# Kernel optimization log

Hardware: AMD Instinct MI355X
Metric: run time of the kernel (lower is better)

The kernel has to match this reference:

```python
import jax, jax.numpy as jnp
import numpy as np

C, W, H = 16, 48, 48
OUTDIMS = 4000
COMPONENTS = 1
BATCH = 128
EPS = 1e-6
INIT_NOISE = 1e-3


def setup_inputs() -> dict:
    key = jax.random.key(0)
    kx, kw, kh, kf = jax.random.split(key, 4)
    x = jax.random.normal(kx, (BATCH, C, W, H), dtype=jnp.float32)
    width = jax.random.normal(kw, (OUTDIMS, 1, W, 1, COMPONENTS), dtype=jnp.float32) * INIT_NOISE
    height = jax.random.normal(kh, (OUTDIMS, 1, 1, H, COMPONENTS), dtype=jnp.float32) * INIT_NOISE
    features = jax.random.normal(kf, (OUTDIMS, C, 1, 1), dtype=jnp.float32) * INIT_NOISE
    bias = jnp.zeros((OUTDIMS,), dtype=jnp.float32)
    return {"x": x, "width": width, "height": height, "features": features, "bias": bias}


def reference(x, width, height, features, bias):
    # normalize width over the w axis (dim 2), height over the h axis (dim 3)
    wn = width / jnp.sqrt(jnp.sum(width * width, axis=2, keepdims=True) + EPS)
    hn = height / jnp.sqrt(jnp.sum(height * height, axis=3, keepdims=True) + EPS)
    # spatial mask: sum of outer products over components -> (outdims, w, h)
    spatial = jnp.sum(wn * hn, axis=4)[:, 0]  # broadcast (n,1,w,1,k)*(n,1,1,h,k)
    feat = features[:, :, 0, 0]  # (outdims, c)
    # y[b,n] = sum_{c,w,h} x[b,c,w,h] * spatial[n,w,h] * feat[n,c]  (same math as
    # x.view(N,-1) @ weight.t() where weight = spatial * features, flattened cwh)
    y = jnp.einsum('bcwh,nwh,nc->bn', x, spatial, feat)
    return y + bias[None, :]
```

## Files before the change

### kernel.cpp

```cpp
#include <hip/hip_runtime.h>
#include <stdint.h>

#define OUTD 4000
#define NPAD 4096
#define CC 16
#define WW 48
#define HH 48
#define BB 128
#define KD 768
#define MD 6144
#define EPSF 1e-6f

#define BM 192
#define BN 128
#define BK 64
#define KSTEPS 12
#define THREADS 512
#define XPB 2304

using short8 = __attribute__((ext_vector_type(8))) short;
using f32x4  = __attribute__((ext_vector_type(4))) float;

static __device__ __forceinline__ unsigned short f2bf(float f) {
  union { float f; unsigned int u; } v; v.f = f;
  unsigned int u = v.u;
  unsigned int r = (u + 0x7FFFu + ((u >> 16) & 1u)) >> 16;
  return (unsigned short)r;
}

__global__ __launch_bounds__(256)
void prep_all(const float* __restrict__ x,
              const float* __restrict__ width,
              const float* __restrict__ height,
              const float* __restrict__ feat,
              unsigned short* __restrict__ A,
              unsigned short* __restrict__ Qt,
              float* __restrict__ wnT) {
  __shared__ float smw[4][WW];
  int bid = blockIdx.x;
  if (bid < XPB) {
    int t = bid * 256 + threadIdx.x;
    int e = t * 8;
    int h0 = e % HH;
    int w = (e / HH) % WW;
    int c = (e / (HH * WW)) % CC;
    int b = e / (HH * WW * CC);
    float4 v0 = *(const float4*)(x + e);
    float4 v1 = *(const float4*)(x + e + 4);
    short8 o;
    o[0] = (short)f2bf(v0.x); o[1] = (short)f2bf(v0.y);
    o[2] = (short)f2bf(v0.z); o[3] = (short)f2bf(v0.w);
    o[4] = (short)f2bf(v1.x); o[5] = (short)f2bf(v1.y);
    o[6] = (short)f2bf(v1.z); o[7] = (short)f2bf(v1.w);
    *(short8*)&A[(size_t)(b * WW + w) * KD + c * HH + h0] = o;
  } else {
    int lane = threadIdx.x & 63;
    int wv = threadIdx.x >> 6;
    int nbase = (bid - XPB) * 4;
    int n = nbase + wv;
    bool valid = (n < OUTD);
    float hv = (valid && lane < HH) ? height[n * HH + lane] : 0.f;
    float wvv = (valid && lane < WW) ? width[n * WW + lane] : 0.f;
    float hs = hv * hv, wsum = wvv * wvv;
    #pragma unroll
    for (int off = 32; off > 0; off >>= 1) {
      hs += __shfl_xor(hs, off);
      wsum += __shfl_xor(wsum, off);
    }
    float hnorm = rsqrtf(hs + EPSF);
    float wnorm = rsqrtf(wsum + EPSF);
    if (lane < WW) smw[wv][lane] = wvv * wnorm;
    if (valid) {
      #pragma unroll
      for (int i = lane; i < KD; i += 64) {
        int c = i / HH, h = i % HH;
        Qt[(size_t)n * KD + i] = f2bf(feat[n * CC + c] * height[n * HH + h] * hnorm);
      }
    } else {
      #pragma unroll
      for (int i = lane; i < KD; i += 64) Qt[(size_t)n * KD + i] = 0;
    }
    __syncthreads();
    if (threadIdx.x < WW) {
      int w = threadIdx.x;
      float4 o = make_float4(smw[0][w], smw[1][w], smw[2][w], smw[3][w]);
      *(float4*)&wnT[w * NPAD + nbase] = o;
    }
  }
}

__global__ __launch_bounds__(THREADS, 2)
void gemm_main(const unsigned short* __restrict__ A,
               const unsigned short* __restrict__ Qt,
               const float* __restrict__ wnT,
               const float* __restrict__ bias,
               float* __restrict__ out) {
  __shared__ unsigned short S[3][(BM + BN) * BK];

  int tid = threadIdx.x;
  int lane = tid & 63;
  int wid = tid >> 6;
  int wm = wid >> 1;
  int wnh = wid & 1;

  int bid = blockIdx.x;
  int xcd = bid & 7;
  int idx = bid >> 3;
  int by = xcd * 4 + (idx & 3);
  int bx = idx >> 2;
  int n0 = bx * BN;
  int m0 = by * BM;

  int rsub = lane >> 3;
  int kswb = ((lane & 7) ^ rsub) * 8;
  const unsigned short* gA[3];
  const unsigned short* gB[2];
  #pragma unroll
  for (int j = 0; j < 3; ++j)
    gA[j] = A + (size_t)(m0 + (wid * 3 + j) * 8 + rsub) * KD + kswb;
  #pragma unroll
  for (int j = 0; j < 2; ++j)
    gB[j] = Qt + (size_t)(n0 + (wid * 2 + j) * 8 + rsub) * KD + kswb;

#define STAGE_A(ks, buf)                                                         \
  { _Pragma("unroll")                                                            \
    for (int j = 0; j < 3; ++j)                                                  \
      __builtin_amdgcn_global_load_lds(                                          \
          (const __attribute__((address_space(1))) void*)(gA[j] + (ks) * BK),    \
          (__attribute__((address_space(3))) void*)(&S[buf][(wid * 3 + j) * 512]), \
          16, 0, 0); }
#define STAGE_B(ks, buf)                                                         \
  { _Pragma("unroll")                                                            \
    for (int j = 0; j < 2; ++j)                                                  \
      __builtin_amdgcn_global_load_lds(                                          \
          (const __attribute__((address_space(1))) void*)(gB[j] + (ks) * BK),    \
          (__attribute__((address_space(3))) void*)(&S[buf][BM * BK + (wid * 2 + j) * 512]), \
          16, 0, 0); }

  int q16 = lane & 15;
  int hi = lane >> 4;
  int q7 = q16 & 7;
  int aofs[2], bofs[2];
  #pragma unroll
  for (int kc = 0; kc < 2; ++kc) {
    aofs[kc] = (wm * 48 + q16) * BK + (((kc * 4 + hi) ^ q7) * 8);
    bofs[kc] = BM * BK + (wnh * 64 + q16) * BK + (((kc * 4 + hi) ^ q7) * 8);
  }

  f32x4 acc[3][4] = {};

  STAGE_A(0, 0); STAGE_B(0, 0);
  STAGE_A(1, 1); STAGE_B(1, 1);
  asm volatile("s_waitcnt vmcnt(5)" ::: "memory");
  __builtin_amdgcn_s_barrier();
  __builtin_amdgcn_sched_barrier(0);

  #pragma unroll
  for (int ks = 0; ks < KSTEPS; ++ks) {
    const unsigned short* sb = &S[ks % 3][0];
    short8 af0, af1, af2;
    #pragma unroll
    for (int kc = 0; kc < 2; ++kc) {
      #pragma unroll
      for (int nh = 0; nh < 2; ++nh) {
        if (nh == 0) {
          af0 = *(const short8*)&sb[aofs[kc]];
          af1 = *(const short8*)&sb[aofs[kc] + 16 * BK];
          af2 = *(const short8*)&sb[aofs[kc] + 32 * BK];
        }
        short8 b0 = *(const short8*)&sb[bofs[kc] + (nh * 2) * 16 * BK];
        short8 b1 = *(const short8*)&sb[bofs[kc] + (nh * 2 + 1) * 16 * BK];
        if (ks + 2 < KSTEPS) {
          if (kc == 0 && nh == 0) STAGE_A(ks + 2, (ks + 2) % 3);
          if (kc == 0 && nh == 1) STAGE_B(ks + 2, (ks + 2) % 3);
        }
        __builtin_amdgcn_s_barrier();
        asm volatile("s_waitcnt lgkmcnt(0)" ::: "memory");
        __builtin_amdgcn_sched_barrier(0);
        __builtin_amdgcn_s_setprio(1);
        acc[0][nh * 2]     = __builtin_amdgcn_mfma_f32_16x16x32_bf16(af0, b0, acc[0][nh * 2], 0, 0, 0);
        acc[1][nh * 2]     = __builtin_amdgcn_mfma_f32_16x16x32_bf16(af1, b0, acc[1][nh * 2], 0, 0, 0);
        acc[2][nh * 2]     = __builtin_amdgcn_mfma_f32_16x16x32_bf16(af2, b0, acc[2][nh * 2], 0, 0, 0);
        acc[0][nh * 2 + 1] = __builtin_amdgcn_mfma_f32_16x16x32_bf16(af0, b1, acc[0][nh * 2 + 1], 0, 0, 0);
        acc[1][nh * 2 + 1] = __builtin_amdgcn_mfma_f32_16x16x32_bf16(af1, b1, acc[1][nh * 2 + 1], 0, 0, 0);
        acc[2][nh * 2 + 1] = __builtin_amdgcn_mfma_f32_16x16x32_bf16(af2, b1, acc[2][nh * 2 + 1], 0, 0, 0);
        __builtin_amdgcn_s_setprio(0);
        if (kc == 1 && nh == 1) {
          if (ks <= KSTEPS - 3)      asm volatile("s_waitcnt vmcnt(5)" ::: "memory");
          else if (ks == KSTEPS - 2) asm volatile("s_waitcnt vmcnt(0)" ::: "memory");
        }
        __builtin_amdgcn_s_barrier();
        __builtin_amdgcn_sched_barrier(0);
      }
    }
  }

  int b = by * 4 + wm;
  #pragma unroll
  for (int ni = 0; ni < 4; ++ni) {
    int ng = n0 + wnh * 64 + ni * 16 + q16;
    float sum = 0.f;
    #pragma unroll
    for (int mi = 0; mi < 3; ++mi) {
      int wbase = mi * 16 + hi * 4;
      f32x4 v = acc[mi][ni];
      #pragma unroll
      for (int r = 0; r < 4; ++r)
        sum += wnT[(wbase + r) * NPAD + ng] * v[r];
    }
    sum += __shfl_xor(sum, 16);
    sum += __shfl_xor(sum, 32);
    if (hi == 0 && ng < OUTD)
      out[(size_t)b * OUTD + ng] = sum + bias[ng];
  }
#undef STAGE_A
#undef STAGE_B
}

extern "C" void kernel_launch(void* const* d_in, const int* in_sizes, int n_in,
                              void* d_out, int out_size, void* d_ws, size_t ws_size,
                              hipStream_t stream) {
  const float* x      = (const float*)d_in[0];
  const float* width  = (const float*)d_in[1];
  const float* height = (const float*)d_in[2];
  const float* feat   = (const float*)d_in[3];
  const float* bias   = (const float*)d_in[4];
  float* out = (float*)d_out;

  char* ws = (char*)d_ws;
  unsigned short* A  = (unsigned short*)ws;
  unsigned short* Qt = (unsigned short*)(ws + 9437184);
  float* wnT         = (float*)(ws + 9437184 + 6291456);

  prep_all<<<dim3(XPB + NPAD / 4), dim3(256), 0, stream>>>(x, width, height, feat, A, Qt, wnT);
  gemm_main<<<dim3(1024), dim3(THREADS), 0, stream>>>(A, Qt, wnT, bias, out);
}
```

Measured before the change: 59.59 us.

## Double GEMM M-tile to 384 and use 4-slot BK=32 pipeline

Doubles the M tile per block from 192 to 384 rows (two batch samples per warp row), halving the grid to 512 blocks so each B tile is reused across more rows. The K loop is restructured into 24 units of BK=32 with a 4-deep LDS ring buffer, prefetching 3 units ahead and using one barrier per unit instead of several. The LDS swizzle and epilogue change to match, and the epilogue writes two output rows per warp. The cost is more accumulator registers (24 f32x4 per wave) and fewer blocks, which risks lower occupancy and a worse tail on 256 CUs.

```diff
diff --git a/kernel.cpp b/kernel.cpp
--- a/kernel.cpp
+++ b/kernel.cpp
@@ -11,10 +11,11 @@
 #define MD 6144
 #define EPSF 1e-6f
 
-#define BM 192
+#define BM 384
 #define BN 128
-#define BK 64
-#define KSTEPS 12
+#define BKU 32
+#define UNITS 24
+#define SLOT_ELEMS ((BM + BN) * BKU)
 #define THREADS 512
 #define XPB 2304
 
@@ -95,7 +96,7 @@
                const float* __restrict__ wnT,
                const float* __restrict__ bias,
                float* __restrict__ out) {
-  __shared__ unsigned short S[3][(BM + BN) * BK];
+  __shared__ unsigned short S[4 * SLOT_ELEMS];
 
   int tid = threadIdx.x;
   int lane = tid & 63;
@@ -105,116 +106,136 @@
 
   int bid = blockIdx.x;
   int xcd = bid & 7;
-  int idx = bid >> 3;
-  int by = xcd * 4 + (idx & 3);
-  int bx = idx >> 2;
+  int i = bid >> 3;
+  int by = xcd * 2 + (i & 1);
+  int bx = i >> 1;
   int n0 = bx * BN;
   int m0 = by * BM;
 
-  int rsub = lane >> 3;
-  int kswb = ((lane & 7) ^ rsub) * 8;
-  const unsigned short* gA[3];
-  const unsigned short* gB[2];
-  #pragma unroll
-  for (int j = 0; j < 3; ++j)
-    gA[j] = A + (size_t)(m0 + (wid * 3 + j) * 8 + rsub) * KD + kswb;
-  #pragma unroll
-  for (int j = 0; j < 2; ++j)
-    gB[j] = Qt + (size_t)(n0 + (wid * 2 + j) * 8 + rsub) * KD + kswb;
-
-#define STAGE_A(ks, buf)                                                         \
-  { _Pragma("unroll")                                                            \
-    for (int j = 0; j < 3; ++j)                                                  \
-      __builtin_amdgcn_global_load_lds(                                          \
-          (const __attribute__((address_space(1))) void*)(gA[j] + (ks) * BK),    \
-          (__attribute__((address_space(3))) void*)(&S[buf][(wid * 3 + j) * 512]), \
-          16, 0, 0); }
-#define STAGE_B(ks, buf)                                                         \
-  { _Pragma("unroll")                                                            \
-    for (int j = 0; j < 2; ++j)                                                  \
-      __builtin_amdgcn_global_load_lds(                                          \
-          (const __attribute__((address_space(1))) void*)(gB[j] + (ks) * BK),    \
-          (__attribute__((address_space(3))) void*)(&S[buf][BM * BK + (wid * 2 + j) * 512]), \
-          16, 0, 0); }
+  int lrow = lane >> 2;
+  int g = lane & 3;
+  int gsw = (g ^ ((lrow >> 1) & 3)) * 8;
+  const unsigned short* gA0 = A + (size_t)(m0 + (wid * 3 + 0) * 16 + lrow) * KD + gsw;
+  const unsigned short* gA1 = A + (size_t)(m0 + (wid * 3 + 1) * 16 + lrow) * KD + gsw;
+  const unsigned short* gA2 = A + (size_t)(m0 + (wid * 3 + 2) * 16 + lrow) * KD + gsw;
+  const unsigned short* gB0 = Qt + (size_t)(n0 + wid * 16 + lrow) * KD + gsw;
+  int aD0 = (wid * 3 + 0) * 512;
+  int aD1 = (wid * 3 + 1) * 512;
+  int aD2 = (wid * 3 + 2) * 512;
+  int bD  = BM * BKU + wid * 512;
+
+#define SLOTB(u) (((u) & 3) * SLOT_ELEMS)
+#define STAGE(u)                                                                  \
+  { __builtin_amdgcn_global_load_lds(                                             \
+        (const __attribute__((address_space(1))) void*)(gA0 + (u) * BKU),         \
+        (__attribute__((address_space(3))) void*)(&S[SLOTB(u) + aD0]), 16, 0, 0); \
+    __builtin_amdgcn_global_load_lds(                                             \
+        (const __attribute__((address_space(1))) void*)(gA1 + (u) * BKU),         \
+        (__attribute__((address_space(3))) void*)(&S[SLOTB(u) + aD1]), 16, 0, 0); \
+    __builtin_amdgcn_global_load_lds(                                             \
+        (const __attribute__((address_space(1))) void*)(gA2 + (u) * BKU),         \
+        (__attribute__((address_space(3))) void*)(&S[SLOTB(u) + aD2]), 16, 0, 0); \
+    __builtin_amdgcn_global_load_lds(                                             \
+        (const __attribute__((address_space(1))) void*)(gB0 + (u) * BKU),         \
+        (__attribute__((address_space(3))) void*)(&S[SLOTB(u) + bD]), 16, 0, 0); }
 
   int q16 = lane & 15;
   int hi = lane >> 4;
-  int q7 = q16 & 7;
-  int aofs[2], bofs[2];
+  int kq = (q16 >> 1) & 3;
+  int aoff = (wm * 96 + q16) * BKU + (hi ^ kq) * 8;
+  int boff = BM * BKU + (wnh * 64 + q16) * BKU + (hi ^ kq) * 8;
+
+  f32x4 acc[6][4] = {};
+
+  STAGE(0); STAGE(1); STAGE(2);
+
   #pragma unroll
-  for (int kc = 0; kc < 2; ++kc) {
-    aofs[kc] = (wm * 48 + q16) * BK + (((kc * 4 + hi) ^ q7) * 8);
-    bofs[kc] = BM * BK + (wnh * 64 + q16) * BK + (((kc * 4 + hi) ^ q7) * 8);
+  for (int u = 0; u < UNITS; ++u) {
+    if (u + 3 < UNITS) STAGE(u + 3);
+    __builtin_amdgcn_sched_barrier(0);
+    if (u <= UNITS - 4)      asm volatile("s_waitcnt vmcnt(12)" ::: "memory");
+    else if (u == UNITS - 3) asm volatile("s_waitcnt vmcnt(8)" ::: "memory");
+    else if (u == UNITS - 2) asm volatile("s_waitcnt vmcnt(4)" ::: "memory");
+    else                     asm volatile("s_waitcnt vmcnt(0)" ::: "memory");
+    __builtin_amdgcn_s_barrier();
+    __builtin_amdgcn_sched_barrier(0);
+
+    const unsigned short* sb = &S[SLOTB(u)];
+    short8 af0 = *(const short8*)&sb[aoff];
+    short8 af1 = *(const short8*)&sb[aoff + 512];
+    short8 af2 = *(const short8*)&sb[aoff + 1024];
+    short8 af3 = *(const short8*)&sb[aoff + 1536];
+    short8 af4 = *(const short8*)&sb[aoff + 2048];
+    short8 af5 = *(const short8*)&sb[aoff + 2560];
+    short8 bf0 = *(const short8*)&sb[boff];
+    short8 bf1 = *(const short8*)&sb[boff + 512];
+    asm volatile("s_waitcnt lgkmcnt(0)" ::: "memory");
+    __builtin_amdgcn_sched_barrier(0);
+    __builtin_amdgcn_s_setprio(1);
+    acc[0][0] = __builtin_amdgcn_mfma_f32_16x16x32_bf16(af0, bf0, acc[0][0], 0, 0, 0);
+    acc[1][0] = __builtin_amdgcn_mfma_f32_16x16x32_bf16(af1, bf0, acc[1][0], 0, 0, 0);
+    acc[2][0] = __builtin_amdgcn_mfma_f32_16x16x32_bf16(af2, bf0, acc[2][0], 0, 0, 0);
+    acc[3][0] = __builtin_amdgcn_mfma_f32_16x16x32_bf16(af3, bf0, acc[3][0], 0, 0, 0);
+    acc[4][0] = __builtin_amdgcn_mfma_f32_16x16x32_bf16(af4, bf0, acc[4][0], 0, 0, 0);
+    acc[5][0] = __builtin_amdgcn_mfma_f32_16x16x32_bf16(af5, bf0, acc[5][0], 0, 0, 0);
+    acc[0][1] = __builtin_amdgcn_mfma_f32_16x16x32_bf16(af0, bf1, acc[0][1], 0, 0, 0);
+    acc[1][1] = __builtin_amdgcn_mfma_f32_16x16x32_bf16(af1, bf1, acc[1][1], 0, 0, 0);
+    acc[2][1] = __builtin_amdgcn_mfma_f32_16x16x32_bf16(af2, bf1, acc[2][1], 0, 0, 0);
+    acc[3][1] = __builtin_amdgcn_mfma_f32_16x16x32_bf16(af3, bf1, acc[3][1], 0, 0, 0);
+    acc[4][1] = __builtin_amdgcn_mfma_f32_16x16x32_bf16(af4, bf1, acc[4][1], 0, 0, 0);
+    acc[5][1] = __builtin_amdgcn_mfma_f32_16x16x32_bf16(af5, bf1, acc[5][1], 0, 0, 0);
+    __builtin_amdgcn_s_setprio(0);
+    __builtin_amdgcn_sched_barrier(0);
+
+    short8 bf2 = *(const short8*)&sb[boff + 1024];
+    short8 bf3 = *(const short8*)&sb[boff + 1536];
+    asm volatile("s_waitcnt lgkmcnt(0)" ::: "memory");
+    __builtin_amdgcn_sched_barrier(0);
+    __builtin_amdgcn_s_setprio(1);
+    acc[0][2] = __builtin_amdgcn_mfma_f32_16x16x32_bf16(af0, bf2, acc[0][2], 0, 0, 0);
+    acc[1][2] = __builtin_amdgcn_mfma_f32_16x16x32_bf16(af1, bf2, acc[1][2], 0, 0, 0);
+    acc[2][2] = __builtin_amdgcn_mfma_f32_16x16x32_bf16(af2, bf2, acc[2][2], 0, 0, 0);
+    acc[3][2] = __builtin_amdgcn_mfma_f32_16x16x32_bf16(af3, bf2, acc[3][2], 0, 0, 0);
+    acc[4][2] = __builtin_amdgcn_mfma_f32_16x16x32_bf16(af4, bf2, acc[4][2], 0, 0, 0);
+    acc[5][2] = __builtin_amdgcn_mfma_f32_16x16x32_bf16(af5, bf2, acc[5][2], 0, 0, 0);
+    acc[0][3] = __builtin_amdgcn_mfma_f32_16x16x32_bf16(af0, bf3, acc[0][3], 0, 0, 0);
+    acc[1][3] = __builtin_amdgcn_mfma_f32_16x16x32_bf16(af1, bf3, acc[1][3], 0, 0, 0);
+    acc[2][3] = __builtin_amdgcn_mfma_f32_16x16x32_bf16(af2, bf3, acc[2][3], 0, 0, 0);
+    acc[3][3] = __builtin_amdgcn_mfma_f32_16x16x32_bf16(af3, bf3, acc[3][3], 0, 0, 0);
+    acc[4][3] = __builtin_amdgcn_mfma_f32_16x16x32_bf16(af4, bf3, acc[4][3], 0, 0, 0);
+    acc[5][3] = __builtin_amdgcn_mfma_f32_16x16x32_bf16(af5, bf3, acc[5][3], 0, 0, 0);
+    __builtin_amdgcn_s_setprio(0);
+    __builtin_amdgcn_s_barrier();
+    __builtin_amdgcn_sched_barrier(0);
   }
 
-  f32x4 acc[3][4] = {};
-
-  STAGE_A(0, 0); STAGE_B(0, 0);
-  STAGE_A(1, 1); STAGE_B(1, 1);
-  asm volatile("s_waitcnt vmcnt(5)" ::: "memory");
-  __builtin_amdgcn_s_barrier();
-  __builtin_amdgcn_sched_barrier(0);
-
-  #pragma unroll
-  for (int ks = 0; ks < KSTEPS; ++ks) {
-    const unsigned short* sb = &S[ks % 3][0];
-    short8 af0, af1, af2;
-    #pragma unroll
-    for (int kc = 0; kc < 2; ++kc) {
-      #pragma unroll
-      for (int nh = 0; nh < 2; ++nh) {
-        if (nh == 0) {
-          af0 = *(const short8*)&sb[aofs[kc]];
-          af1 = *(const short8*)&sb[aofs[kc] + 16 * BK];
-          af2 = *(const short8*)&sb[aofs[kc] + 32 * BK];
-        }
-        short8 b0 = *(const short8*)&sb[bofs[kc] + (nh * 2) * 16 * BK];
-        short8 b1 = *(const short8*)&sb[bofs[kc] + (nh * 2 + 1) * 16 * BK];
-        if (ks + 2 < KSTEPS) {
-          if (kc == 0 && nh == 0) STAGE_A(ks + 2, (ks + 2) % 3);
-          if (kc == 0 && nh == 1) STAGE_B(ks + 2, (ks + 2) % 3);
-        }
-        __builtin_amdgcn_s_barrier();
-        asm volatile("s_waitcnt lgkmcnt(0)" ::: "memory");
-        __builtin_amdgcn_sched_barrier(0);
-        __builtin_amdgcn_s_setprio(1);
-        acc[0][nh * 2]     = __builtin_amdgcn_mfma_f32_16x16x32_bf16(af0, b0, acc[0][nh * 2], 0, 0, 0);
-        acc[1][nh * 2]     = __builtin_amdgcn_mfma_f32_16x16x32_bf16(af1, b0, acc[1][nh * 2], 0, 0, 0);
-        acc[2][nh * 2]     = __builtin_amdgcn_mfma_f32_16x16x32_bf16(af2, b0, acc[2][nh * 2], 0, 0, 0);
-        acc[0][nh * 2 + 1] = __builtin_amdgcn_mfma_f32_16x16x32_bf16(af0, b1, acc[0][nh * 2 + 1], 0, 0, 0);
-        acc[1][nh * 2 + 1] = __builtin_amdgcn_mfma_f32_16x16x32_bf16(af1, b1, acc[1][nh * 2 + 1], 0, 0, 0);
-        acc[2][nh * 2 + 1] = __builtin_amdgcn_mfma_f32_16x16x32_bf16(af2, b1, acc[2][nh * 2 + 1], 0, 0, 0);
-        __builtin_amdgcn_s_setprio(0);
-        if (kc == 1 && nh == 1) {
-          if (ks <= KSTEPS - 3)      asm volatile("s_waitcnt vmcnt(5)" ::: "memory");
-          else if (ks == KSTEPS - 2) asm volatile("s_waitcnt vmcnt(0)" ::: "memory");
-        }
-        __builtin_amdgcn_s_barrier();
-        __builtin_amdgcn_sched_barrier(0);
-      }
-    }
-  }
-
-  int b = by * 4 + wm;
+  int b0 = by * 8 + wm * 2;
   #pragma unroll
   for (int ni = 0; ni < 4; ++ni) {
     int ng = n0 + wnh * 64 + ni * 16 + q16;
-    float sum = 0.f;
+    float s0 = 0.f, s1 = 0.f;
     #pragma unroll
     for (int mi = 0; mi < 3; ++mi) {
       int wbase = mi * 16 + hi * 4;
-      f32x4 v = acc[mi][ni];
+      f32x4 va = acc[mi][ni];
+      f32x4 vb = acc[mi + 3][ni];
       #pragma unroll
-      for (int r = 0; r < 4; ++r)
-        sum += wnT[(wbase + r) * NPAD + ng] * v[r];
-    }
-    sum += __shfl_xor(sum, 16);
-    sum += __shfl_xor(sum, 32);
-    if (hi == 0 && ng < OUTD)
-      out[(size_t)b * OUTD + ng] = sum + bias[ng];
+      for (int r = 0; r < 4; ++r) {
+        float t = wnT[(wbase + r) * NPAD + ng];
+        s0 += t * va[r];
+        s1 += t * vb[r];
+      }
+    }
+    s0 += __shfl_xor(s0, 16); s0 += __shfl_xor(s0, 32);
+    s1 += __shfl_xor(s1, 16); s1 += __shfl_xor(s1, 32);
+    if (hi == 0 && ng < OUTD) {
+      float bv = bias[ng];
+      out[(size_t)b0 * OUTD + ng] = s0 + bv;
+      out[(size_t)(b0 + 1) * OUTD + ng] = s1 + bv;
+    }
   }
-#undef STAGE_A
-#undef STAGE_B
+#undef STAGE
+#undef SLOTB
 }
 
 extern "C" void kernel_launch(void* const* d_in, const int* in_sizes, int n_in,
@@ -233,5 +254,5 @@
   float* wnT         = (float*)(ws + 9437184 + 6291456);
 
   prep_all<<<dim3(XPB + NPAD / 4), dim3(256), 0, stream>>>(x, width, height, feat, A, Qt, wnT);
-  gemm_main<<<dim3(1024), dim3(THREADS), 0, stream>>>(A, Qt, wnT, bias, out);
-}
+  gemm_main<<<dim3(512), dim3(THREADS), 0, stream>>>(A, Qt, wnT, bias, out);
+}
```

After: 56.89 us. -4.5%, faster.
